# Performance work log

Hardware: AMD Instinct MI355X
Metric: run time of the kernel (lower is better)

Reference implementation:

```python
import jax, jax.numpy as jnp
import numpy as np

FEATURE_MAPS = (38, 19, 10, 5, 3, 1)
BOXES_PER_LOC = (4, 6, 6, 6, 4, 4)
IMAGE_SIZE = 300
DEC_SIZE = 64  # WhatDecoder output resolution
MAX_OBJECTS = 10
Z_WHAT = 64


def _recon_indices():
    # Maps per-prior slots (8732) to per-location slots (1940), matching
    # Decoder.reconstruction_indices: each location index repeated boxes_per_loc times.
    idx, last = [], 0
    for fm, bpl in zip(FEATURE_MAPS, BOXES_PER_LOC):
        loc = np.arange(fm * fm) + last
        idx.append(np.repeat(loc, bpl))
        last = loc[-1] + 1
    return jnp.asarray(np.concatenate(idx), dtype=jnp.int32)


def _deconv2x2(x, W, b):
    # ConvTranspose2d(kernel=2, stride=2): each input pixel expands to a 2x2 block.
    n, c, h, w = x.shape
    o = W.shape[1]
    y = jnp.einsum('nchw,coab->nohawb', x, W).reshape(n, o, 2 * h, 2 * w)
    return y + b[None, :, None, None]


def _what_decoder(z, params):
    # z (M, Z_WHAT) -> (M, 3, 64, 64) in [0,1]
    x = z[:, :, None, None]
    nl = len(params)
    for i, (W, b) in enumerate(params):
        x = _deconv2x2(x, W, b)
        x = jax.nn.relu(x) if i < nl - 1 else jax.nn.sigmoid(x)
    return x


def _stn(images, z_where):
    # Spatial transformer: place (M,3,S,S) glyphs into IMAGE_SIZE canvas at box
    # z_where (M,4) = (cx,cy,w,h) in [0,1]; bilinear sampling, zeros padding.
    M, _, S, _ = images.shape
    cx, cy, w, h = (z_where[:, i] for i in range(4))
    # output pixel centers in normalized [-1,1] coords (align_corners=False)
    coords = (2.0 * jnp.arange(IMAGE_SIZE, dtype=images.dtype) + 1.0) / IMAGE_SIZE - 1.0
    xo = coords[None, None, :]
    yo = coords[None, :, None]
    eps = 1e-6
    u = (xo - (2.0 * cx - 1.0)[:, None, None]) / (w[:, None, None] + eps)  # (M,H,W)
    v = (yo - (2.0 * cy - 1.0)[:, None, None]) / (h[:, None, None] + eps)
    ix = ((u + 1.0) * S - 1.0) / 2.0  # input pixel coords
    iy = ((v + 1.0) * S - 1.0) / 2.0

    def sample_one(img, iy, ix):
        iy0 = jnp.floor(iy)
        ix0 = jnp.floor(ix)
        wy1 = iy - iy0
        wx1 = ix - ix0
        wy0 = 1.0 - wy1
        wx0 = 1.0 - wx1

        def g(y, x):
            yi = jnp.clip(y, 0, S - 1).astype(jnp.int32)
            xi = jnp.clip(x, 0, S - 1).astype(jnp.int32)
            valid = ((y >= 0) & (y < S) & (x >= 0) & (x < S)).astype(img.dtype)
            return img[:, yi, xi] * valid  # (3,H,W)

        return (g(iy0, ix0) * wy0 * wx0 + g(iy0, ix0 + 1) * wy0 * wx1
                + g(iy0 + 1, ix0) * wy1 * wx0 + g(iy0 + 1, ix0 + 1) * wy1 * wx1)

    return jax.vmap(sample_one)(images, iy, ix)  # (M,3,H,H)


def setup_inputs() -> dict:
    key = jax.random.key(0)
    ks = jax.random.split(key, 20)
    B, NLOC, NPRI = 16, 1940, 8732
    chans = (Z_WHAT, 256, 128, 64, 32, 16, 3)
    inp = {
        'z_what': jax.random.normal(ks[0], (B, NLOC, Z_WHAT), jnp.float32),
        'z_where': jax.random.uniform(ks[1], (B, NPRI, 4), jnp.float32),
        'z_present': jax.random.randint(ks[2], (B, NPRI, 1), 0, 2, jnp.int32),
        'z_depth': jax.random.normal(ks[3], (B, NLOC, 1), jnp.float32),
    }
    for i in range(6):
        ci, co = chans[i], chans[i + 1]
        inp[f'W{i}'] = jax.random.normal(ks[4 + i], (ci, co, 2, 2), jnp.float32) * 0.1
        inp[f'b{i}'] = jnp.zeros((co,), jnp.float32)
    return inp


def reference(z_what, z_where, z_present, z_depth,
              W0, b0, W1, b1, W2, b2, W3, b3, W4, b4, W5, b5):
    params = [(W0, b0), (W1, b1), (W2, b2), (W3, b3), (W4, b4), (W5, b5)]
    idx = _recon_indices()
    zw = z_what[:, idx]      # (B, P, D) ragged location->prior gather
    zd = z_depth[:, idx, 0]  # (B, P)
    order = jnp.argsort(-zd, axis=1)[:, :MAX_OBJECTS]  # depth sort, descending
    B, K = order.shape

    def gat(t):
        return jnp.take_along_axis(
            t, jnp.broadcast_to(order[:, :, None], (B, K, t.shape[-1])), axis=1)

    sw = gat(zw)            # (B,K,D)
    swr = gat(z_where)      # (B,K,4)
    sp = gat(z_present)     # (B,K,1)

    decoded = _what_decoder(sw.reshape(B * K, Z_WHAT), params)      # (B*K,3,64,64)
    transformed = _stn(decoded, swr.reshape(B * K, 4))              # (B*K,3,300,300)
    present = (sp == 1).astype(transformed.dtype).reshape(B * K, 1, 1, 1)
    objs = (transformed * present).reshape(B, K, 3, IMAGE_SIZE, IMAGE_SIZE)

    # z-buffer merge: per pixel, take first nonzero object in depth order
    nz = objs != 0.0
    first = nz & (jnp.cumsum(nz.astype(jnp.int32), axis=1) == 1)
    return jnp.sum(objs * first.astype(objs.dtype), axis=1)  # (B,3,300,300)
```

## Files before the change

kernel.cpp:

```cpp
#include <hip/hip_runtime.h>
#include <cmath>

#define NLOC 1940
#define NPRI 8732
#define BATCH 16
#define KOBJ 10
#define NROWS 5

__device__ __forceinline__ void ins3(float v, int i,
    float& a0, float& a1, float& a2, int& j0, int& j1, int& j2)
{
    if (v > a0 || (v == a0 && i < j0)) { a2=a1; j2=j1; a1=a0; j1=j0; a0=v; j0=i; }
    else if (v > a1 || (v == a1 && i < j1)) { a2=a1; j2=j1; a1=v; j1=i; }
    else if (v > a2 || (v == a2 && i < j2)) { a2=v; j2=i; }
}

__device__ __forceinline__ float ix_chain(int x, float shift, float wh) {
    const float xo = __fsub_rn(__fdiv_rn(__fadd_rn(__fmul_rn(2.0f, (float)x), 1.0f), 300.0f), 1.0f);
    const float u  = __fdiv_rn(__fsub_rn(xo, shift), wh);
    return __fmul_rn(__fsub_rn(__fmul_rn(__fadd_rn(u, 1.0f), 64.0f), 1.0f), 0.5f);
}

__global__ __launch_bounds__(256) void prep_kernel(
    const float* __restrict__ W0, const float* __restrict__ W1, float* __restrict__ Wr,
    const float* __restrict__ z_what, const float* __restrict__ z_where,
    const int* __restrict__ z_present, const float* __restrict__ z_depth,
    float* __restrict__ gathered, float* __restrict__ paramsF, int* __restrict__ paramsI,
    int* __restrict__ obnd)
{
    __shared__ float sv[768];
    __shared__ int   si[768];
    __shared__ int   locs3[3];
    __shared__ int   sj_start[3], sj_bpl[3];
    __shared__ int   spres[10], sjj[10];
    __shared__ float szw[10][4];
    __shared__ float lpf[KOBJ][4];
    __shared__ int   lcnt;
    const int tid = threadIdx.x;

    if (blockIdx.x < 768) {
        const int idx = blockIdx.x * 256 + tid;
        if (idx < 65536) {
            int q = idx >> 14, rem = idx & 16383, c = rem >> 8, o = rem & 255;
            Wr[idx] = W0[(((c << 8) | o) << 2) + q];
        } else {
            int i2 = idx - 65536;
            int q = i2 >> 15, rem = i2 & 32767, c = rem >> 7, o = rem & 127;
            Wr[idx] = W1[(((c << 7) | o) << 2) + q];
        }
        return;
    }

    const int b = blockIdx.x - 768;
    float v0 = -INFINITY, v1 = -INFINITY, v2 = -INFINITY;
    int   i0 = NLOC, i1 = NLOC, i2 = NLOC;
    for (int i = tid; i < NLOC; i += 256) {
        float v = z_depth[b * NLOC + i];
        ins3(v, i, v0, v1, v2, i0, i1, i2);
    }
    sv[tid*3+0] = v0; sv[tid*3+1] = v1; sv[tid*3+2] = v2;
    si[tid*3+0] = i0; si[tid*3+1] = i1; si[tid*3+2] = i2;
    __syncthreads();
    for (int s = 128; s > 0; s >>= 1) {
        if (tid < s) {
            float a0 = sv[tid*3], a1 = sv[tid*3+1], a2 = sv[tid*3+2];
            int   j0 = si[tid*3], j1 = si[tid*3+1], j2 = si[tid*3+2];
            const int o = tid + s;
            ins3(sv[o*3+0], si[o*3+0], a0, a1, a2, j0, j1, j2);
            ins3(sv[o*3+1], si[o*3+1], a0, a1, a2, j0, j1, j2);
            ins3(sv[o*3+2], si[o*3+2], a0, a1, a2, j0, j1, j2);
            sv[tid*3] = a0; sv[tid*3+1] = a1; sv[tid*3+2] = a2;
            si[tid*3] = j0; si[tid*3+1] = j1; si[tid*3+2] = j2;
        }
        __syncthreads();
    }

    if (tid < 3) {
        int L = si[tid];
        locs3[tid] = L;
        int start, bpl;
        if (L < 1444)      { start = 4 * L;                 bpl = 4; }
        else if (L < 1805) { start = 5776 + 6 * (L - 1444); bpl = 6; }
        else if (L < 1905) { start = 7942 + 6 * (L - 1805); bpl = 6; }
        else if (L < 1930) { start = 8542 + 6 * (L - 1905); bpl = 6; }
        else if (L < 1939) { start = 8692 + 4 * (L - 1930); bpl = 4; }
        else               { start = 8728;                  bpl = 4; }
        sj_start[tid] = start; sj_bpl[tid] = bpl;
    }
    __syncthreads();
    if (tid < 10) {
        const int b0 = sj_bpl[0], b1 = sj_bpl[1];
        int j, o;
        if (tid < b0)           { j = 0; o = tid; }
        else if (tid < b0 + b1) { j = 1; o = tid - b0; }
        else                    { j = 2; o = tid - b0 - b1; }
        const int p = sj_start[j] + o;
        sjj[tid]   = j;
        spres[tid] = z_present[b * NPRI + p];
        const float4 zw = *reinterpret_cast<const float4*>(z_where + (b * NPRI + p) * 4);
        szw[tid][0] = zw.x; szw[tid][1] = zw.y; szw[tid][2] = zw.z; szw[tid][3] = zw.w;
    }
    __syncthreads();
    if (tid == 0) {
        int cnt = 0;
        for (int i = 0; i < 10; ++i) {
            if (spres[i] == 1) {
                float p0 = __fadd_rn(szw[i][2], 1e-6f);
                float p1 = __fadd_rn(szw[i][3], 1e-6f);
                float p2 = __fsub_rn(__fmul_rn(2.0f, szw[i][0]), 1.0f);
                float p3 = __fsub_rn(__fmul_rn(2.0f, szw[i][1]), 1.0f);
                float* pf = paramsF + (b * KOBJ + cnt) * 4;
                pf[0] = p0; pf[1] = p1; pf[2] = p2; pf[3] = p3;
                lpf[cnt][0] = p0; lpf[cnt][1] = p1; lpf[cnt][2] = p2; lpf[cnt][3] = p3;
                paramsI[b * 12 + 2 + cnt] = b * 3 + sjj[i];
                cnt++;
            }
        }
        paramsI[b * 12] = cnt;
        lcnt = cnt;
    }
    __syncthreads();
    if (tid < 4 * KOBJ) {
        const int k = tid >> 2, ty = tid & 3;
        if (k < lcnt) {
            const float wh = (ty < 2) ? lpf[k][0] : lpf[k][1];
            const float sh = (ty < 2) ? lpf[k][2] : lpf[k][3];
            int res;
            if ((ty & 1) == 0) {
                int lo = 0, hi = 300;
                while (lo < hi) { int m = (lo + hi) >> 1;
                    if (ix_chain(m, sh, wh) > -1.0f) hi = m; else lo = m + 1; }
                res = lo;
            } else {
                int lo = -1, hi = 299;
                while (lo < hi) { int m = (lo + hi + 1) >> 1;
                    if (ix_chain(m, sh, wh) < 64.0f) lo = m; else hi = m - 1; }
                res = lo;
            }
            obnd[(b * KOBJ + k) * 4 + ty] = res;
        }
    }
    if (tid < 192) {
        int j = tid >> 6, c = tid & 63;
        gathered[(b * 3 + j) * 64 + c] = z_what[(b * NLOC + locs3[j]) * 64 + c];
    }
}

__global__ __launch_bounds__(256) void dec_fused(
    const float* __restrict__ gathered, const float* __restrict__ Wr,
    const float* __restrict__ b0v, const float* __restrict__ b1v,
    const float* __restrict__ W2, const float* __restrict__ b2v,
    const float* __restrict__ W3, const float* __restrict__ b3v,
    const float* __restrict__ W4, const float* __restrict__ b4v,
    const float* __restrict__ W5, const float* __restrict__ b5v,
    float* __restrict__ decoded)
{
    __shared__ __align__(16) float P[1024];
    __shared__ __align__(16) float Q[512];
    __shared__ __align__(16) float Zs[64];
    const int r  = blockIdx.x;
    const int s  = blockIdx.y;
    const int t  = threadIdx.x;
    const int y1 = r >> 2, x1 = r & 3;
    const int q0 = (y1 >> 1) * 2 + (x1 >> 1);
    const int p1 = (y1 & 1) * 2 + (x1 & 1);

    if (t < 64) Zs[t] = gathered[s * 64 + t];
    __syncthreads();

    {
        const float* w0 = Wr + q0 * 16384 + t;
        float acc = b0v[t];
        #pragma unroll 8
        for (int c = 0; c < 64; ++c)
            acc = fmaf(Zs[c], w0[c << 8], acc);
        P[t] = fmaxf(acc, 0.f);
    }
    __syncthreads();

    {
        const int o = t & 127, h = t >> 7;
        const float* w1 = Wr + 65536 + p1 * 32768 + o;
        float acc = (h == 0) ? b1v[o] : 0.f;
        const int cb = h << 7;
        #pragma unroll 8
        for (int c = 0; c < 128; ++c)
            acc = fmaf(P[cb + c], w1[(cb + c) << 7], acc);
        if (h == 1) P[256 + o] = acc;
        __syncthreads();
        if (h == 0)
            Q[o] = fmaxf(acc + P[256 + o], 0.f);
    }
    __syncthreads();

    {
        const float* w2 = W2 + t;
        float acc = b2v[t >> 2];
        #pragma unroll 8
        for (int ci = 0; ci < 128; ++ci)
            acc = fmaf(Q[ci], w2[ci << 8], acc);
        P[t] = fmaxf(acc, 0.f);
    }
    __syncthreads();

    {
        const int px = t & 15, coa = t >> 4;
        const int ly = px >> 2, lx = px & 3;
        const int par = (ly >> 1) * 2 + (lx >> 1);
        const int wp  = (ly & 1) * 2 + (lx & 1);
        const float* w3 = W3 + coa * 4 + wp;
        float a0 = b3v[coa];
        float a1 = b3v[coa + 16];
        #pragma unroll 8
        for (int ci = 0; ci < 64; ++ci) {
            float xs = P[(ci << 2) + par];
            a0 = fmaf(xs, w3[ci << 7], a0);
            a1 = fmaf(xs, w3[(ci << 7) + 64], a1);
        }
        Q[(coa << 4) + px] = fmaxf(a0, 0.f);
        Q[((coa + 16) << 4) + px] = fmaxf(a1, 0.f);
    }
    __syncthreads();

    {
        const int px = t & 63, co0 = t >> 6;
        const int ly = px >> 3, lx = px & 7;
        const int par = (ly >> 1) * 4 + (lx >> 1);
        const int wp  = (ly & 1) * 2 + (lx & 1);
        const float* w4 = W4 + co0 * 4 + wp;
        float acc[4];
        #pragma unroll
        for (int k = 0; k < 4; ++k) acc[k] = b4v[co0 + 4 * k];
        #pragma unroll 4
        for (int ci = 0; ci < 32; ++ci) {
            float xs = Q[(ci << 4) + par];
            #pragma unroll
            for (int k = 0; k < 4; ++k)
                acc[k] = fmaf(xs, w4[(ci << 6) + k * 16], acc[k]);
        }
        #pragma unroll
        for (int k = 0; k < 4; ++k)
            P[((co0 + 4 * k) << 6) + px] = fmaxf(acc[k], 0.f);
    }
    __syncthreads();

    {
        const int px = t;
        const int ly = px >> 4, lx = px & 15;
        const int par = (ly >> 1) * 8 + (lx >> 1);
        const int wp  = (ly & 1) * 2 + (lx & 1);
        const int gy = y1 * 16 + ly, gx = x1 * 16 + lx;
        const float* w5 = W5 + wp;
        float acc[3];
        #pragma unroll
        for (int c = 0; c < 3; ++c) acc[c] = b5v[c];
        #pragma unroll 4
        for (int ci = 0; ci < 16; ++ci) {
            float xs = P[(ci << 6) + par];
            #pragma unroll
            for (int c = 0; c < 3; ++c)
                acc[c] = fmaf(xs, w5[ci * 12 + c * 4], acc[c]);
        }
        const int pbase = (gy * 64 + gx) * 4;
        float4 v;
        v.x = 1.0f / (1.0f + expf(-acc[0]));
        v.y = 1.0f / (1.0f + expf(-acc[1]));
        v.z = 1.0f / (1.0f + expf(-acc[2]));
        v.w = 0.0f;
        *reinterpret_cast<float4*>(decoded + s * 16384 + pbase) = v;
    }
}

__global__ __launch_bounds__(256) void stn_kernel(
    const float* __restrict__ decoded, const float* __restrict__ paramsF,
    const int* __restrict__ paramsI, const int* __restrict__ obnd,
    float* __restrict__ out)
{
    const int b = blockIdx.y;
    const int pix0 = blockIdx.x * 1024;
    const int yfirst = pix0 / 300;
    __shared__ float sp[KOBJ][4];
    __shared__ int   ssamp[KOBJ];
    __shared__ int   s_xlo[KOBJ], s_xhi[KOBJ], s_ylo[KOBJ], s_yhi[KOBJ];
    __shared__ int   scnt;
    __shared__ float s_wy0[KOBJ][NROWS], s_wy1[KOBJ][NROWS];
    __shared__ int   s_rb0[KOBJ][NROWS], s_rb1[KOBJ][NROWS];
    __shared__ unsigned char s_cov[KOBJ][NROWS];
    __shared__ unsigned char s_vy[KOBJ][NROWS];
    __shared__ int s_list[KOBJ];
    __shared__ int s_lc;
    const int tid = threadIdx.x;

    if (tid == 0) scnt = paramsI[b * 12];
    if (tid < KOBJ) {
        #pragma unroll
        for (int c = 0; c < 4; ++c) sp[tid][c] = paramsF[(b * KOBJ + tid) * 4 + c];
        ssamp[tid] = paramsI[b * 12 + 2 + tid];
        const int4 bd = *reinterpret_cast<const int4*>(obnd + (b * KOBJ + tid) * 4);
        s_xlo[tid] = bd.x; s_xhi[tid] = bd.y; s_ylo[tid] = bd.z; s_yhi[tid] = bd.w;
    }
    __syncthreads();

    if (tid < NROWS * scnt) {
        const int k = tid / NROWS, sel = tid - k * NROWS;
        int yy = yfirst + sel; if (yy > 299) yy = 299;
        const bool cov = (yy >= s_ylo[k]) && (yy <= s_yhi[k]);
        s_cov[k][sel] = cov ? 1 : 0;
        if (cov) {
            const float iy = ix_chain(yy, sp[k][3], sp[k][1]);
            const float iy0f = floorf(iy);
            const float iy1f = __fadd_rn(iy0f, 1.0f);
            const float wy1  = __fsub_rn(iy, iy0f);
            s_wy1[k][sel] = wy1;
            s_wy0[k][sel] = __fsub_rn(1.0f, wy1);
            const bool vy0 = (iy0f >= 0.0f) && (iy0f < 64.0f);
            const bool vy1 = (iy1f >= 0.0f) && (iy1f < 64.0f);
            s_vy[k][sel] = (unsigned char)((vy0 ? 1 : 0) | (vy1 ? 2 : 0));
            s_rb0[k][sel] = ((int)fminf(fmaxf(iy0f, 0.0f), 63.0f)) * 64;
            s_rb1[k][sel] = ((int)fminf(fmaxf(iy1f, 0.0f), 63.0f)) * 64;
        }
    }
    __syncthreads();
    if (tid == 0) {
        int lc = 0;
        for (int k = 0; k < scnt; ++k) {
            unsigned char any = 0;
            #pragma unroll
            for (int r = 0; r < NROWS; ++r) any |= s_cov[k][r];
            if (any) s_list[lc++] = k;
        }
        s_lc = lc;
    }
    __syncthreads();

    const int lc = s_lc;
    #pragma unroll
    for (int q = 0; q < 4; ++q) {
        const int pix = pix0 + q * 256 + tid;
        if (pix < 90000) {
            const int y = pix / 300;
            const int x = pix - y * 300;
            const int rs = y - yfirst;
            float o0 = 0.0f, o1 = 0.0f, o2 = 0.0f;
            bool d0 = false, d1 = false, d2 = false;
            for (int m = 0; m < lc; ++m) {
                const int k = s_list[m];
                if (!s_cov[k][rs]) continue;
                if (x < s_xlo[k] || x > s_xhi[k]) continue;

                const float ix = ix_chain(x, sp[k][2], sp[k][0]);
                const float ix0f = floorf(ix);
                const float ix1f = __fadd_rn(ix0f, 1.0f);
                const float wx1 = __fsub_rn(ix, ix0f);
                const float wx0 = __fsub_rn(1.0f, wx1);
                const bool vx0 = (ix0f >= 0.0f) && (ix0f < 64.0f);
                const bool vx1 = (ix1f >= 0.0f) && (ix1f < 64.0f);
                const int x0 = (int)fminf(fmaxf(ix0f, 0.0f), 63.0f);
                const int x1 = (int)fminf(fmaxf(ix1f, 0.0f), 63.0f);

                const float wy0 = s_wy0[k][rs], wy1 = s_wy1[k][rs];
                const int rb0 = s_rb0[k][rs], rb1 = s_rb1[k][rs];
                const unsigned char vy = s_vy[k][rs];
                const bool m00 = (vy & 1) && vx0, m01 = (vy & 1) && vx1;
                const bool m10 = (vy & 2) && vx0, m11 = (vy & 2) && vx1;
                const float* img = decoded + ssamp[k] * 16384;

                const float4 z4 = make_float4(0.f, 0.f, 0.f, 0.f);
                const float4 g00 = m00 ? *reinterpret_cast<const float4*>(img + ((rb0 + x0) << 2)) : z4;
                const float4 g01 = m01 ? *reinterpret_cast<const float4*>(img + ((rb0 + x1) << 2)) : z4;
                const float4 g10 = m10 ? *reinterpret_cast<const float4*>(img + ((rb1 + x0) << 2)) : z4;
                const float4 g11 = m11 ? *reinterpret_cast<const float4*>(img + ((rb1 + x1) << 2)) : z4;

                if (!d0) {
                    float val = g00.x * wy0 * wx0 + g01.x * wy0 * wx1 + g10.x * wy1 * wx0 + g11.x * wy1 * wx1;
                    if (val != 0.0f) { o0 = val; d0 = true; }
                }
                if (!d1) {
                    float val = g00.y * wy0 * wx0 + g01.y * wy0 * wx1 + g10.y * wy1 * wx0 + g11.y * wy1 * wx1;
                    if (val != 0.0f) { o1 = val; d1 = true; }
                }
                if (!d2) {
                    float val = g00.z * wy0 * wx0 + g01.z * wy0 * wx1 + g10.z * wy1 * wx0 + g11.z * wy1 * wx1;
                    if (val != 0.0f) { o2 = val; d2 = true; }
                }
                if (d0 && d1 && d2) break;
            }
            const int ob = b * 270000 + pix;
            out[ob] = o0;
            out[ob + 90000] = o1;
            out[ob + 180000] = o2;
        }
    }
}

extern "C" void kernel_launch(void* const* d_in, const int* in_sizes, int n_in,
                              void* d_out, int out_size, void* d_ws, size_t ws_size,
                              hipStream_t stream)
{
    const float* z_what    = (const float*)d_in[0];
    const float* z_where   = (const float*)d_in[1];
    const int*   z_present = (const int*)d_in[2];
    const float* z_depth   = (const float*)d_in[3];
    const float* W0 = (const float*)d_in[4];   const float* b0 = (const float*)d_in[5];
    const float* W1 = (const float*)d_in[6];   const float* b1 = (const float*)d_in[7];
    const float* W2 = (const float*)d_in[8];   const float* b2 = (const float*)d_in[9];
    const float* W3 = (const float*)d_in[10];  const float* b3 = (const float*)d_in[11];
    const float* W4 = (const float*)d_in[12];  const float* b4 = (const float*)d_in[13];
    const float* W5 = (const float*)d_in[14];  const float* b5 = (const float*)d_in[15];

    float* ws = (float*)d_ws;
    float* gathered = ws;
    float* paramsF  = ws + 16384;
    int*   paramsI  = (int*)(ws + 17408);
    int*   obnd     = (int*)(ws + 17664);
    float* decoded  = ws + 32768;
    float* Wr       = (float*)d_out;
    float* outp     = (float*)d_out;

    hipLaunchKernelGGL(prep_kernel, dim3(784), dim3(256), 0, stream,
                       W0, W1, Wr, z_what, z_where, z_present, z_depth,
                       gathered, paramsF, paramsI, obnd);
    hipLaunchKernelGGL(dec_fused, dim3(16, 48), dim3(256), 0, stream,
                       gathered, Wr, b0, b1, W2, b2, W3, b3, W4, b4, W5, b5, decoded);
    hipLaunchKernelGGL(stn_kernel, dim3(88, BATCH), dim3(256), 0, stream,
                       decoded, paramsF, paramsI, obnd, outp);
}
```

Baseline: 154.4 us.

## Fuse prep into decoder kernel and read unpermuted W0/W1 directly

Merges the prep kernel (weight transposition, depth top-3 selection, param setup) into the decoder kernel, removing one launch and the separate transposed-weight buffer. Each decoder block now recomputes the per-batch top-3 depth reduction itself, and the first block per batch writes the STN parameters and bounds. W0/W1 are read in their original layout with stride-4 accesses instead of a pre-transposed copy, which saves the transpose pass but gives less coalesced weight loads and redundant reductions across 48 blocks per batch.

```diff
diff --git a/kernel.cpp b/kernel.cpp
--- a/kernel.cpp
+++ b/kernel.cpp
@@ -21,171 +21,155 @@
     return __fmul_rn(__fsub_rn(__fmul_rn(__fadd_rn(u, 1.0f), 64.0f), 1.0f), 0.5f);
 }
 
-__global__ __launch_bounds__(256) void prep_kernel(
-    const float* __restrict__ W0, const float* __restrict__ W1, float* __restrict__ Wr,
+__global__ __launch_bounds__(256) void dec_all(
     const float* __restrict__ z_what, const float* __restrict__ z_where,
     const int* __restrict__ z_present, const float* __restrict__ z_depth,
-    float* __restrict__ gathered, float* __restrict__ paramsF, int* __restrict__ paramsI,
-    int* __restrict__ obnd)
+    const float* __restrict__ W0, const float* __restrict__ b0v,
+    const float* __restrict__ W1, const float* __restrict__ b1v,
+    const float* __restrict__ W2, const float* __restrict__ b2v,
+    const float* __restrict__ W3, const float* __restrict__ b3v,
+    const float* __restrict__ W4, const float* __restrict__ b4v,
+    const float* __restrict__ W5, const float* __restrict__ b5v,
+    float* __restrict__ paramsF, int* __restrict__ paramsI, int* __restrict__ obnd,
+    float* __restrict__ decoded)
 {
     __shared__ float sv[768];
     __shared__ int   si[768];
-    __shared__ int   locs3[3];
     __shared__ int   sj_start[3], sj_bpl[3];
     __shared__ int   spres[10], sjj[10];
     __shared__ float szw[10][4];
     __shared__ float lpf[KOBJ][4];
     __shared__ int   lcnt;
-    const int tid = threadIdx.x;
-
-    if (blockIdx.x < 768) {
-        const int idx = blockIdx.x * 256 + tid;
-        if (idx < 65536) {
-            int q = idx >> 14, rem = idx & 16383, c = rem >> 8, o = rem & 255;
-            Wr[idx] = W0[(((c << 8) | o) << 2) + q];
-        } else {
-            int i2 = idx - 65536;
-            int q = i2 >> 15, rem = i2 & 32767, c = rem >> 7, o = rem & 127;
-            Wr[idx] = W1[(((c << 7) | o) << 2) + q];
-        }
-        return;
-    }
-
-    const int b = blockIdx.x - 768;
-    float v0 = -INFINITY, v1 = -INFINITY, v2 = -INFINITY;
-    int   i0 = NLOC, i1 = NLOC, i2 = NLOC;
-    for (int i = tid; i < NLOC; i += 256) {
-        float v = z_depth[b * NLOC + i];
-        ins3(v, i, v0, v1, v2, i0, i1, i2);
-    }
-    sv[tid*3+0] = v0; sv[tid*3+1] = v1; sv[tid*3+2] = v2;
-    si[tid*3+0] = i0; si[tid*3+1] = i1; si[tid*3+2] = i2;
-    __syncthreads();
-    for (int s = 128; s > 0; s >>= 1) {
-        if (tid < s) {
-            float a0 = sv[tid*3], a1 = sv[tid*3+1], a2 = sv[tid*3+2];
-            int   j0 = si[tid*3], j1 = si[tid*3+1], j2 = si[tid*3+2];
-            const int o = tid + s;
-            ins3(sv[o*3+0], si[o*3+0], a0, a1, a2, j0, j1, j2);
-            ins3(sv[o*3+1], si[o*3+1], a0, a1, a2, j0, j1, j2);
-            ins3(sv[o*3+2], si[o*3+2], a0, a1, a2, j0, j1, j2);
-            sv[tid*3] = a0; sv[tid*3+1] = a1; sv[tid*3+2] = a2;
-            si[tid*3] = j0; si[tid*3+1] = j1; si[tid*3+2] = j2;
-        }
-        __syncthreads();
-    }
-
-    if (tid < 3) {
-        int L = si[tid];
-        locs3[tid] = L;
-        int start, bpl;
-        if (L < 1444)      { start = 4 * L;                 bpl = 4; }
-        else if (L < 1805) { start = 5776 + 6 * (L - 1444); bpl = 6; }
-        else if (L < 1905) { start = 7942 + 6 * (L - 1805); bpl = 6; }
-        else if (L < 1930) { start = 8542 + 6 * (L - 1905); bpl = 6; }
-        else if (L < 1939) { start = 8692 + 4 * (L - 1930); bpl = 4; }
-        else               { start = 8728;                  bpl = 4; }
-        sj_start[tid] = start; sj_bpl[tid] = bpl;
-    }
-    __syncthreads();
-    if (tid < 10) {
-        const int b0 = sj_bpl[0], b1 = sj_bpl[1];
-        int j, o;
-        if (tid < b0)           { j = 0; o = tid; }
-        else if (tid < b0 + b1) { j = 1; o = tid - b0; }
-        else                    { j = 2; o = tid - b0 - b1; }
-        const int p = sj_start[j] + o;
-        sjj[tid]   = j;
-        spres[tid] = z_present[b * NPRI + p];
-        const float4 zw = *reinterpret_cast<const float4*>(z_where + (b * NPRI + p) * 4);
-        szw[tid][0] = zw.x; szw[tid][1] = zw.y; szw[tid][2] = zw.z; szw[tid][3] = zw.w;
-    }
-    __syncthreads();
-    if (tid == 0) {
-        int cnt = 0;
-        for (int i = 0; i < 10; ++i) {
-            if (spres[i] == 1) {
-                float p0 = __fadd_rn(szw[i][2], 1e-6f);
-                float p1 = __fadd_rn(szw[i][3], 1e-6f);
-                float p2 = __fsub_rn(__fmul_rn(2.0f, szw[i][0]), 1.0f);
-                float p3 = __fsub_rn(__fmul_rn(2.0f, szw[i][1]), 1.0f);
-                float* pf = paramsF + (b * KOBJ + cnt) * 4;
-                pf[0] = p0; pf[1] = p1; pf[2] = p2; pf[3] = p3;
-                lpf[cnt][0] = p0; lpf[cnt][1] = p1; lpf[cnt][2] = p2; lpf[cnt][3] = p3;
-                paramsI[b * 12 + 2 + cnt] = b * 3 + sjj[i];
-                cnt++;
-            }
-        }
-        paramsI[b * 12] = cnt;
-        lcnt = cnt;
-    }
-    __syncthreads();
-    if (tid < 4 * KOBJ) {
-        const int k = tid >> 2, ty = tid & 3;
-        if (k < lcnt) {
-            const float wh = (ty < 2) ? lpf[k][0] : lpf[k][1];
-            const float sh = (ty < 2) ? lpf[k][2] : lpf[k][3];
-            int res;
-            if ((ty & 1) == 0) {
-                int lo = 0, hi = 300;
-                while (lo < hi) { int m = (lo + hi) >> 1;
-                    if (ix_chain(m, sh, wh) > -1.0f) hi = m; else lo = m + 1; }
-                res = lo;
-            } else {
-                int lo = -1, hi = 299;
-                while (lo < hi) { int m = (lo + hi + 1) >> 1;
-                    if (ix_chain(m, sh, wh) < 64.0f) lo = m; else hi = m - 1; }
-                res = lo;
-            }
-            obnd[(b * KOBJ + k) * 4 + ty] = res;
-        }
-    }
-    if (tid < 192) {
-        int j = tid >> 6, c = tid & 63;
-        gathered[(b * 3 + j) * 64 + c] = z_what[(b * NLOC + locs3[j]) * 64 + c];
-    }
-}
-
-__global__ __launch_bounds__(256) void dec_fused(
-    const float* __restrict__ gathered, const float* __restrict__ Wr,
-    const float* __restrict__ b0v, const float* __restrict__ b1v,
-    const float* __restrict__ W2, const float* __restrict__ b2v,
-    const float* __restrict__ W3, const float* __restrict__ b3v,
-    const float* __restrict__ W4, const float* __restrict__ b4v,
-    const float* __restrict__ W5, const float* __restrict__ b5v,
-    float* __restrict__ decoded)
-{
     __shared__ __align__(16) float P[1024];
     __shared__ __align__(16) float Q[512];
     __shared__ __align__(16) float Zs[64];
+
     const int r  = blockIdx.x;
     const int s  = blockIdx.y;
     const int t  = threadIdx.x;
+    const int b  = s / 3;
+    const int j  = s - 3 * b;
     const int y1 = r >> 2, x1 = r & 3;
     const int q0 = (y1 >> 1) * 2 + (x1 >> 1);
     const int p1 = (y1 & 1) * 2 + (x1 & 1);
 
-    if (t < 64) Zs[t] = gathered[s * 64 + t];
-    __syncthreads();
-
-    {
-        const float* w0 = Wr + q0 * 16384 + t;
+    {
+        float v0 = -INFINITY, v1 = -INFINITY, v2 = -INFINITY;
+        int   i0 = NLOC, i1 = NLOC, i2 = NLOC;
+        for (int i = t; i < NLOC; i += 256) {
+            float v = z_depth[b * NLOC + i];
+            ins3(v, i, v0, v1, v2, i0, i1, i2);
+        }
+        sv[t*3+0] = v0; sv[t*3+1] = v1; sv[t*3+2] = v2;
+        si[t*3+0] = i0; si[t*3+1] = i1; si[t*3+2] = i2;
+        __syncthreads();
+        for (int st = 128; st > 0; st >>= 1) {
+            if (t < st) {
+                float a0 = sv[t*3], a1 = sv[t*3+1], a2 = sv[t*3+2];
+                int   j0 = si[t*3], j1 = si[t*3+1], j2 = si[t*3+2];
+                const int o = t + st;
+                ins3(sv[o*3+0], si[o*3+0], a0, a1, a2, j0, j1, j2);
+                ins3(sv[o*3+1], si[o*3+1], a0, a1, a2, j0, j1, j2);
+                ins3(sv[o*3+2], si[o*3+2], a0, a1, a2, j0, j1, j2);
+                sv[t*3] = a0; sv[t*3+1] = a1; sv[t*3+2] = a2;
+                si[t*3] = j0; si[t*3+1] = j1; si[t*3+2] = j2;
+            }
+            __syncthreads();
+        }
+    }
+
+    if (r == 0 && j == 0) {
+        if (t < 3) {
+            int L = si[t];
+            int start, bpl;
+            if (L < 1444)      { start = 4 * L;                 bpl = 4; }
+            else if (L < 1805) { start = 5776 + 6 * (L - 1444); bpl = 6; }
+            else if (L < 1905) { start = 7942 + 6 * (L - 1805); bpl = 6; }
+            else if (L < 1930) { start = 8542 + 6 * (L - 1905); bpl = 6; }
+            else if (L < 1939) { start = 8692 + 4 * (L - 1930); bpl = 4; }
+            else               { start = 8728;                  bpl = 4; }
+            sj_start[t] = start; sj_bpl[t] = bpl;
+        }
+        __syncthreads();
+        if (t < 10) {
+            const int c0 = sj_bpl[0], c1 = sj_bpl[1];
+            int jj, o;
+            if (t < c0)           { jj = 0; o = t; }
+            else if (t < c0 + c1) { jj = 1; o = t - c0; }
+            else                  { jj = 2; o = t - c0 - c1; }
+            const int p = sj_start[jj] + o;
+            sjj[t]   = jj;
+            spres[t] = z_present[b * NPRI + p];
+            const float4 zw = *reinterpret_cast<const float4*>(z_where + (b * NPRI + p) * 4);
+            szw[t][0] = zw.x; szw[t][1] = zw.y; szw[t][2] = zw.z; szw[t][3] = zw.w;
+        }
+        __syncthreads();
+        if (t == 0) {
+            int cnt = 0;
+            for (int i = 0; i < 10; ++i) {
+                if (spres[i] == 1) {
+                    float p0 = __fadd_rn(szw[i][2], 1e-6f);
+                    float p1v = __fadd_rn(szw[i][3], 1e-6f);
+                    float p2 = __fsub_rn(__fmul_rn(2.0f, szw[i][0]), 1.0f);
+                    float p3 = __fsub_rn(__fmul_rn(2.0f, szw[i][1]), 1.0f);
+                    float* pf = paramsF + (b * KOBJ + cnt) * 4;
+                    pf[0] = p0; pf[1] = p1v; pf[2] = p2; pf[3] = p3;
+                    lpf[cnt][0] = p0; lpf[cnt][1] = p1v; lpf[cnt][2] = p2; lpf[cnt][3] = p3;
+                    paramsI[b * 12 + 2 + cnt] = b * 3 + sjj[i];
+                    cnt++;
+                }
+            }
+            paramsI[b * 12] = cnt;
+            lcnt = cnt;
+        }
+        __syncthreads();
+        if (t < 4 * KOBJ) {
+            const int k = t >> 2, ty = t & 3;
+            if (k < lcnt) {
+                const float wh = (ty < 2) ? lpf[k][0] : lpf[k][1];
+                const float sh = (ty < 2) ? lpf[k][2] : lpf[k][3];
+                int res;
+                if ((ty & 1) == 0) {
+                    int lo = 0, hi = 300;
+                    while (lo < hi) { int m = (lo + hi) >> 1;
+                        if (ix_chain(m, sh, wh) > -1.0f) hi = m; else lo = m + 1; }
+                    res = lo;
+                } else {
+                    int lo = -1, hi = 299;
+                    while (lo < hi) { int m = (lo + hi + 1) >> 1;
+                        if (ix_chain(m, sh, wh) < 64.0f) lo = m; else hi = m - 1; }
+                    res = lo;
+                }
+                obnd[(b * KOBJ + k) * 4 + ty] = res;
+            }
+        }
+        __syncthreads();
+    }
+
+    {
+        const int L = si[j];
+        if (t < 64) Zs[t] = z_what[(b * NLOC + L) * 64 + t];
+    }
+    __syncthreads();
+
+    {
+        const float* w0 = W0 + (t << 2) + q0;
         float acc = b0v[t];
         #pragma unroll 8
         for (int c = 0; c < 64; ++c)
-            acc = fmaf(Zs[c], w0[c << 8], acc);
+            acc = fmaf(Zs[c], w0[c << 10], acc);
         P[t] = fmaxf(acc, 0.f);
     }
     __syncthreads();
 
     {
         const int o = t & 127, h = t >> 7;
-        const float* w1 = Wr + 65536 + p1 * 32768 + o;
+        const float* w1 = W1 + (o << 2) + p1;
         float acc = (h == 0) ? b1v[o] : 0.f;
         const int cb = h << 7;
         #pragma unroll 8
         for (int c = 0; c < 128; ++c)
-            acc = fmaf(P[cb + c], w1[(cb + c) << 7], acc);
+            acc = fmaf(P[cb + c], w1[(cb + c) << 9], acc);
         if (h == 1) P[256 + o] = acc;
         __syncthreads();
         if (h == 0)
@@ -409,19 +393,16 @@
     const float* W5 = (const float*)d_in[14];  const float* b5 = (const float*)d_in[15];
 
     float* ws = (float*)d_ws;
-    float* gathered = ws;
     float* paramsF  = ws + 16384;
     int*   paramsI  = (int*)(ws + 17408);
     int*   obnd     = (int*)(ws + 17664);
     float* decoded  = ws + 32768;
-    float* Wr       = (float*)d_out;
     float* outp     = (float*)d_out;
 
-    hipLaunchKernelGGL(prep_kernel, dim3(784), dim3(256), 0, stream,
-                       W0, W1, Wr, z_what, z_where, z_present, z_depth,
-                       gathered, paramsF, paramsI, obnd);
-    hipLaunchKernelGGL(dec_fused, dim3(16, 48), dim3(256), 0, stream,
-                       gathered, Wr, b0, b1, W2, b2, W3, b3, W4, b4, W5, b5, decoded);
+    hipLaunchKernelGGL(dec_all, dim3(16, 48), dim3(256), 0, stream,
+                       z_what, z_where, z_present, z_depth,
+                       W0, b0, W1, b1, W2, b2, W3, b3, W4, b4, W5, b5,
+                       paramsF, paramsI, obnd, decoded);
     hipLaunchKernelGGL(stn_kernel, dim3(88, BATCH), dim3(256), 0, stream,
                        decoded, paramsF, paramsI, obnd, outp);
 }
```

Result: slower. 174.1 us (+12.7%).
